# Performance work log

Measured on AMD Instinct MI355X. Metric: run time of the kernel, lower is better.

The kernel has to match this reference:

```python
import jax, jax.numpy as jnp
import numpy as np

B, L, H = 16, 4096, 768

def setup_inputs() -> dict:
    key = jax.random.key(0)
    k1, k2 = jax.random.split(key)
    sequence_output = jax.random.normal(k1, (B, L, H), dtype=jnp.float32)
    # sorted segment ids: each wordpiece position maps to a token index in [0, L)
    wordpiece_to_token = jnp.sort(
        jax.random.randint(k2, (B, L), 0, L, dtype=jnp.int32), axis=-1)
    return {"sequence_output": sequence_output,
            "wordpiece_to_token": wordpiece_to_token}

def reference(sequence_output, wordpiece_to_token):
    # For each (batch, token j): output[b, j] = sum of sequence_output[b, p]
    # over wordpieces p assigned to token j. Tokens with no wordpieces stay 0,
    # matching torch.zeros_like initialization in the original.
    num_tokens = sequence_output.shape[1]
    def per_example(x, seg):  # x: [L, H], seg: [L]
        return jax.ops.segment_sum(x, seg, num_segments=num_tokens)
    return jax.vmap(per_example)(sequence_output, wordpiece_to_token)
```

## Files before the change

kernel.cpp:

```cpp
#include <hip/hip_runtime.h>

#define BB 16
#define LL 4096
#define H4 192
#define SP 4104

typedef float nf4 __attribute__((ext_vector_type(4)));

__global__ __launch_bounds__(256) void bounds_kernel(
    const int* __restrict__ seg, int* __restrict__ starts) {
    int b = blockIdx.x >> 4;
    int p = ((blockIdx.x & 15) << 8) | threadIdx.x;
    const int* __restrict__ sb = seg + (b << 12);
    int* __restrict__ st = starts + b * SP;

    int cur  = sb[p];
    int prev = (p == 0) ? -1 : sb[p - 1];
    for (int j = prev + 1; j <= cur; ++j) st[j] = p;
    if (p == LL - 1)
        for (int j = cur + 1; j <= LL; ++j) st[j] = LL;
}

__global__ __launch_bounds__(256) void segsum_bounds_kernel(
    const float4* __restrict__ x, const int* __restrict__ starts,
    float4* __restrict__ out) {
    int gtid = blockIdx.x * blockDim.x + threadIdx.x;
    int wave = gtid >> 6;
    int lane = gtid & 63;
    int b = wave >> 12;
    int j = wave & (LL - 1);

    const int* __restrict__ st = starts + b * SP + j;
    int s = st[0];
    int e = st[1];

    float4 a0 = make_float4(0.f, 0.f, 0.f, 0.f);
    float4 a1 = a0, a2 = a0;

    const float4* xb = x + (size_t)b * LL * H4;
    for (int p = s; p < e; ++p) {
        const float4* row = xb + (size_t)p * H4 + lane;
        float4 v0 = row[0];
        float4 vA = row[64];
        float4 vB = row[128];
        a0.x += v0.x; a0.y += v0.y; a0.z += v0.z; a0.w += v0.w;
        a1.x += vA.x; a1.y += vA.y; a1.z += vA.z; a1.w += vA.w;
        a2.x += vB.x; a2.y += vB.y; a2.z += vB.z; a2.w += vB.w;
    }

    nf4* orow = (nf4*)(out + (size_t)wave * H4 + lane);
    nf4 n0 = {a0.x, a0.y, a0.z, a0.w};
    nf4 n1 = {a1.x, a1.y, a1.z, a1.w};
    nf4 n2 = {a2.x, a2.y, a2.z, a2.w};
    __builtin_nontemporal_store(n0, orow);
    __builtin_nontemporal_store(n1, orow + 64);
    __builtin_nontemporal_store(n2, orow + 128);
}

__global__ __launch_bounds__(256) void segsum_fused_kernel(
    const float4* __restrict__ x, const int* __restrict__ seg,
    float4* __restrict__ out) {
    int gtid = blockIdx.x * blockDim.x + threadIdx.x;
    int wave = gtid >> 6;
    int lane = gtid & 63;
    int b = wave >> 12;
    int j = wave & (LL - 1);

    const int* __restrict__ sb = seg + ((size_t)b << 12);

    int v1 = sb[lane << 6];
    unsigned long long ms = __ballot(v1 >= j);
    unsigned long long me = __ballot(v1 > j);

    int s, e;
    if (ms & 1ull) {
        s = 0;
    } else {
        int f = ms ? (__ffsll((unsigned long long)ms) - 1) : 64;
        int base = ((f - 1) << 6) + 1;
        int p2 = base + lane;
        int v2 = (p2 < LL) ? sb[p2] : 0x7fffffff;
        unsigned long long m2 = __ballot(v2 >= j);
        s = base + __ffsll(m2) - 1;
    }
    if (me & 1ull) {
        e = 0;
    } else {
        int f = me ? (__ffsll((unsigned long long)me) - 1) : 64;
        int base = ((f - 1) << 6) + 1;
        int p2 = base + lane;
        int v2 = (p2 < LL) ? sb[p2] : 0x7fffffff;
        unsigned long long m2 = __ballot(v2 > j);
        e = base + __ffsll(m2) - 1;
    }

    float4 a0 = make_float4(0.f, 0.f, 0.f, 0.f);
    float4 a1 = a0, a2 = a0;

    const float4* xb = x + (size_t)b * LL * H4;
    for (int p = s; p < e; ++p) {
        const float4* row = xb + (size_t)p * H4 + lane;
        float4 v0 = row[0];
        float4 vA = row[64];
        float4 vB = row[128];
        a0.x += v0.x; a0.y += v0.y; a0.z += v0.z; a0.w += v0.w;
        a1.x += vA.x; a1.y += vA.y; a1.z += vA.z; a1.w += vA.w;
        a2.x += vB.x; a2.y += vB.y; a2.z += vB.z; a2.w += vB.w;
    }

    float4* orow = out + (size_t)wave * H4 + lane;
    orow[0]   = a0;
    orow[64]  = a1;
    orow[128] = a2;
}

extern "C" void kernel_launch(void* const* d_in, const int* in_sizes, int n_in,
                              void* d_out, int out_size, void* d_ws, size_t ws_size,
                              hipStream_t stream) {
    const float* x   = (const float*)d_in[0];
    const int*   seg = (const int*)d_in[1];
    float* out = (float*)d_out;

    size_t need = (size_t)BB * SP * sizeof(int);
    if (d_ws != nullptr && ws_size >= need) {
        int* starts = (int*)d_ws;
        bounds_kernel<<<BB * 16, 256, 0, stream>>>(seg, starts);
        segsum_bounds_kernel<<<(BB * LL) / 4, 256, 0, stream>>>(
            (const float4*)x, starts, (float4*)out);
    } else {
        segsum_fused_kernel<<<(BB * LL) / 4, 256, 0, stream>>>(
            (const float4*)x, seg, (float4*)out);
    }
}
```

Measured before the change: 343.2 us.

## Process eight tokens per wave with streaming segment walk and prefetch

Each wave now owns a chunk of eight consecutive output tokens and walks the wordpiece range for that chunk once. It reads segment ids to detect token boundaries, flushes the accumulator at each boundary, and zero-fills empty tokens. The next row is loaded one iteration ahead to hide memory latency. This cuts the wave count eightfold and amortizes the bounds lookups, but makes each wave's work serial and uneven, lowers parallelism, and drops the nontemporal stores.

```diff
diff --git a/kernel.cpp b/kernel.cpp
--- a/kernel.cpp
+++ b/kernel.cpp
@@ -4,8 +4,8 @@
 #define LL 4096
 #define H4 192
 #define SP 4104
-
-typedef float nf4 __attribute__((ext_vector_type(4)));
+#define TT 8
+#define LOG2T 3
 
 __global__ __launch_bounds__(256) void bounds_kernel(
     const int* __restrict__ seg, int* __restrict__ starts) {
@@ -21,40 +21,64 @@
         for (int j = cur + 1; j <= LL; ++j) st[j] = LL;
 }
 
-__global__ __launch_bounds__(256) void segsum_bounds_kernel(
-    const float4* __restrict__ x, const int* __restrict__ starts,
-    float4* __restrict__ out) {
+__global__ __launch_bounds__(256) void segsum_stream_kernel(
+    const float4* __restrict__ x, const int* __restrict__ seg,
+    const int* __restrict__ starts, float4* __restrict__ out) {
     int gtid = blockIdx.x * blockDim.x + threadIdx.x;
     int wave = gtid >> 6;
     int lane = gtid & 63;
-    int b = wave >> 12;
-    int j = wave & (LL - 1);
+    int b    = wave >> (12 - LOG2T);
+    int j0   = (wave & ((LL >> LOG2T) - 1)) << LOG2T;
 
-    const int* __restrict__ st = starts + b * SP + j;
-    int s = st[0];
-    int e = st[1];
+    const int* __restrict__ st = starts + b * SP;
+    int s = st[j0];
+    int e = st[j0 + TT];
 
-    float4 a0 = make_float4(0.f, 0.f, 0.f, 0.f);
-    float4 a1 = a0, a2 = a0;
+    const float4* __restrict__ xb = x + (size_t)b * (LL * H4);
+    const int*    __restrict__ sb = seg + (b << 12);
+    float4*       __restrict__ ob = out + ((size_t)(b << 12) + j0) * H4 + lane;
 
-    const float4* xb = x + (size_t)b * LL * H4;
-    for (int p = s; p < e; ++p) {
-        const float4* row = xb + (size_t)p * H4 + lane;
-        float4 v0 = row[0];
-        float4 vA = row[64];
-        float4 vB = row[128];
-        a0.x += v0.x; a0.y += v0.y; a0.z += v0.z; a0.w += v0.w;
-        a1.x += vA.x; a1.y += vA.y; a1.z += vA.z; a1.w += vA.w;
-        a2.x += vB.x; a2.y += vB.y; a2.z += vB.z; a2.w += vB.w;
+    const float4 z = make_float4(0.f, 0.f, 0.f, 0.f);
+    float4 a0 = z, a1 = z, a2 = z;
+    int cur = j0;
+
+    float4 n0 = z, n1 = z, n2 = z;
+    int tn = 0;
+    if (s < e) {
+        const float4* r = xb + (size_t)s * H4 + lane;
+        n0 = r[0]; n1 = r[64]; n2 = r[128];
+        tn = sb[s];
     }
 
-    nf4* orow = (nf4*)(out + (size_t)wave * H4 + lane);
-    nf4 n0 = {a0.x, a0.y, a0.z, a0.w};
-    nf4 n1 = {a1.x, a1.y, a1.z, a1.w};
-    nf4 n2 = {a2.x, a2.y, a2.z, a2.w};
-    __builtin_nontemporal_store(n0, orow);
-    __builtin_nontemporal_store(n1, orow + 64);
-    __builtin_nontemporal_store(n2, orow + 128);
+    for (int p = s; p < e; ++p) {
+        float4 c0 = n0, c1 = n1, c2 = n2;
+        int t = tn;
+        int pn = (p + 1 < e) ? (p + 1) : p;
+        const float4* r = xb + (size_t)pn * H4 + lane;
+        n0 = r[0]; n1 = r[64]; n2 = r[128];
+        tn = sb[pn];
+
+        if (t != cur) {
+            float4* orow = ob + (size_t)(cur - j0) * H4;
+            orow[0] = a0; orow[64] = a1; orow[128] = a2;
+            for (int g = cur + 1; g < t; ++g) {
+                float4* og = ob + (size_t)(g - j0) * H4;
+                og[0] = z; og[64] = z; og[128] = z;
+            }
+            a0 = z; a1 = z; a2 = z;
+            cur = t;
+        }
+        a0.x += c0.x; a0.y += c0.y; a0.z += c0.z; a0.w += c0.w;
+        a1.x += c1.x; a1.y += c1.y; a1.z += c1.z; a1.w += c1.w;
+        a2.x += c2.x; a2.y += c2.y; a2.z += c2.z; a2.w += c2.w;
+    }
+
+    float4* orow = ob + (size_t)(cur - j0) * H4;
+    orow[0] = a0; orow[64] = a1; orow[128] = a2;
+    for (int g = cur + 1; g < j0 + TT; ++g) {
+        float4* og = ob + (size_t)(g - j0) * H4;
+        og[0] = z; og[64] = z; og[128] = z;
+    }
 }
 
 __global__ __launch_bounds__(256) void segsum_fused_kernel(
@@ -125,8 +149,8 @@
     if (d_ws != nullptr && ws_size >= need) {
         int* starts = (int*)d_ws;
         bounds_kernel<<<BB * 16, 256, 0, stream>>>(seg, starts);
-        segsum_bounds_kernel<<<(BB * LL) / 4, 256, 0, stream>>>(
-            (const float4*)x, starts, (float4*)out);
+        segsum_stream_kernel<<<(BB * (LL >> LOG2T)) / 4, 256, 0, stream>>>(
+            (const float4*)x, seg, starts, (float4*)out);
     } else {
         segsum_fused_kernel<<<(BB * LL) / 4, 256, 0, stream>>>(
             (const float4*)x, seg, (float4*)out);
```

New measurement: 343.6 us. No clear change (+0.1%).
